# Kernel optimization log

Hardware: AMD Instinct MI355X
Metric: run time of the kernel (lower is better)

## Reference

```python
import jax, jax.numpy as jnp
import numpy as np

EPS = 1e-5

def setup_inputs() -> dict:
    key = jax.random.key(0)
    ks = jax.random.split(key, 8)
    B, T, D, S = 8, 4096, 1024, 64
    return {
        "x": jax.random.normal(ks[0], (B, T, D), dtype=jnp.float32),
        "time_decay": jax.random.normal(ks[1], (S,), dtype=jnp.float32) * 0.1 - 0.5,
        "time_first": jax.random.normal(ks[2], (S,), dtype=jnp.float32) * 0.1,
        "W_key": jax.random.normal(ks[3], (S, D), dtype=jnp.float32) * 0.02,
        "W_value": jax.random.normal(ks[4], (S, D), dtype=jnp.float32) * 0.02,
        "W_output": jax.random.normal(ks[5], (D, S), dtype=jnp.float32) * 0.02,
        "W_shift": jax.random.normal(ks[6], (D, D), dtype=jnp.float32) * 0.02,
        "shift_gate": jnp.ones((D,), dtype=jnp.float32),
        "ln_w": jnp.ones((D,), dtype=jnp.float32),
        "ln_b": jnp.zeros((D,), dtype=jnp.float32),
    }


def _forward(x, time_decay, time_first, W_key, W_value, W_output, W_shift, shift_gate, ln_w, ln_b):
    B, T, D = x.shape
    S = time_decay.shape[0]
    # --- token shift: rotate sequence by shift_len, project, gated blend ---
    shift_len = max(1, int(T * 0.5))
    x_cat = jnp.concatenate([x[:, shift_len:], x[:, :-shift_len]], axis=1)  # (B,T,D)
    gate = jax.nn.sigmoid(shift_gate)
    x_shift = jnp.einsum('btd,ed->bte', x_cat, W_shift) * gate + x * (1.0 - gate)
    # --- layernorm (torch: biased variance, eps=1e-5) ---
    mu = jnp.mean(x_shift, axis=-1, keepdims=True)
    var = jnp.mean(jnp.square(x_shift - mu), axis=-1, keepdims=True)
    xn = (x_shift - mu) * jax.lax.rsqrt(var + EPS) * ln_w + ln_b
    # --- key/value projections and per-step wkv (fully vectorized) ---
    k = jnp.einsum('btd,sd->bts', xn, W_key)    # (B,T,S)
    v = jnp.einsum('btd,sd->bts', xn, W_value)  # (B,T,S)
    wkv = jnp.exp(-jnp.exp(time_first) * jax.nn.sigmoid(k)) * v  # (B,T,S)
    # --- linear recurrence: state = state*w + wkv_t, scanned over T ---
    w = jnp.exp(time_decay)  # (S,)
    def step(state, wkv_t):
        state = state * w + wkv_t
        return state, state
    init = jnp.zeros((B, S), dtype=x.dtype)
    last_state, states = jax.lax.scan(step, init, jnp.swapaxes(wkv, 0, 1))  # states: (T,B,S)
    states = jnp.swapaxes(states, 0, 1)  # (B,T,S)
    # --- batched output projection (applied per-step in torch; same math) ---
    output = jnp.einsum('bts,ds->btd', states, W_output)  # (B,T,D)
    return output, last_state


def reference(x, time_decay, time_first, W_key, W_value, W_output, W_shift, shift_gate, ln_w, ln_b):
    out, last_state = _forward(x, time_decay, time_first, W_key, W_value, W_output, W_shift, shift_gate, ln_w, ln_b)
    return out, jax.lax.stop_gradient(last_state)
```

## Files before the change

kernel.cpp:

```cpp
#include <hip/hip_runtime.h>
#include <stdint.h>

#define B_ 8
#define T_ 4096
#define D_ 1024
#define S_ 64
#define N_ 32768
#define OUT_ELEMS 33554432
#define NCHK 128
#define CHKL 32

typedef __attribute__((ext_vector_type(8))) short bf16x8;
typedef __attribute__((ext_vector_type(8))) unsigned short u16x8;
typedef __attribute__((ext_vector_type(4))) float f32x4;

__device__ __forceinline__ uint16_t f2bf(float f) {
    union { float f; uint32_t u; } v; v.f = f;
    uint32_t r = v.u + 0x7FFFu + ((v.u >> 16) & 1u);
    return (uint16_t)(r >> 16);
}
__device__ __forceinline__ float bf2f(uint16_t h) {
    union { uint32_t u; float f; } v; v.u = ((uint32_t)h) << 16;
    return v.f;
}

#define GLOAD_LDS16(gp, lp)                                             \
    __builtin_amdgcn_global_load_lds(                                   \
        (const __attribute__((address_space(1))) void*)(gp),            \
        (__attribute__((address_space(3))) void*)(lp), 16, 0, 0)

__global__ void prep(const float* __restrict__ x,
                     const float* __restrict__ Wsf, const float* __restrict__ Wkf,
                     const float* __restrict__ Wvf, const float* __restrict__ Wof,
                     const float* __restrict__ sg, const float* __restrict__ tf,
                     const float* __restrict__ lnw, const float* __restrict__ lnb,
                     uint16_t* __restrict__ xb, uint16_t* __restrict__ Wsb,
                     uint16_t* __restrict__ Wkvb, uint16_t* __restrict__ Wob,
                     float* __restrict__ gbuf, float* __restrict__ efirst,
                     float* __restrict__ ucvec)
{
    __shared__ float red[4];
    const int blk = blockIdx.x, tid = threadIdx.x;
    if (blk < 2048) {
        for (int i = blk * 256 + tid; i < OUT_ELEMS / 4; i += 2048 * 256) {
            float4 v = ((const float4*)x)[i];
            ushort4 o;
            o.x = f2bf(v.x); o.y = f2bf(v.y); o.z = f2bf(v.z); o.w = f2bf(v.w);
            ((ushort4*)xb)[i] = o;
        }
        return;
    }
    if (blk < 3298) {
        int i = (blk - 2048) * 256 + tid;
        const float* src; uint16_t* dst; int j; bool fold = false;
        if (i < 262144) { src = Wsf; dst = Wsb; j = i; }
        else if (i < 278528) { src = Wkf; dst = Wkvb; j = i - 262144; fold = true; }
        else if (i < 294912) { src = Wvf; dst = Wkvb + 65536; j = i - 278528; fold = true; }
        else if (i < 311296) { src = Wof; dst = Wob; j = i - 294912; }
        else if (i < 311552) {
            j = i - 311296;
            float4 v = ((const float4*)sg)[j];
            float4 g;
            g.x = 1.f / (1.f + __expf(-v.x)); g.y = 1.f / (1.f + __expf(-v.y));
            g.z = 1.f / (1.f + __expf(-v.z)); g.w = 1.f / (1.f + __expf(-v.w));
            ((float4*)gbuf)[j] = g;
            return;
        } else if (i < 311568) {
            j = i - 311552;
            float4 v = ((const float4*)tf)[j];
            float4 e;
            e.x = __expf(v.x); e.y = __expf(v.y); e.z = __expf(v.z); e.w = __expf(v.w);
            ((float4*)efirst)[j] = e;
            return;
        } else return;
        float4 v = ((const float4*)src)[j];
        if (fold) {
            float4 l = ((const float4*)lnw)[j & 255];
            v.x *= l.x; v.y *= l.y; v.z *= l.z; v.w *= l.w;
        }
        ushort4 o;
        o.x = f2bf(v.x); o.y = f2bf(v.y); o.z = f2bf(v.z); o.w = f2bf(v.w);
        ((ushort4*)dst)[j] = o;
        return;
    }
    {
        int b2 = blk - 3298;
        int which = b2 >> 6, s = b2 & 63;
        const float* W = (which < 2) ? Wkf : Wvf;
        const float* L = (which & 1) ? lnb : lnw;
        float4 wv = ((const float4*)W)[s * 256 + tid];
        float4 lv = ((const float4*)L)[tid];
        float p = wv.x * lv.x + wv.y * lv.y + wv.z * lv.z + wv.w * lv.w;
#pragma unroll
        for (int off = 32; off; off >>= 1) p += __shfl_xor(p, off);
        if ((tid & 63) == 0) red[tid >> 6] = p;
        __syncthreads();
        if (tid == 0) ucvec[which * 64 + s] = red[0] + red[1] + red[2] + red[3];
    }
}

__global__ __launch_bounds__(512, 2) void k1_shift_gemm(
    const uint16_t* __restrict__ xb, const uint16_t* __restrict__ Wsb,
    const float* __restrict__ gbuf, uint16_t* __restrict__ xs)
{
    __shared__ char sh[131072];

    const int tid = threadIdx.x;
    const int w = tid >> 6, lane = tid & 63, quad = lane >> 4, l16 = lane & 15;
    const int wm = w >> 2, wn = w & 3;
    const int w8 = w * 8;

    const int lin = blockIdx.x;
    const int idx = lin >> 3;
    const int nt = idx & 3;
    const int mt = (lin & 7) * 16 + (idx >> 2);
    const int m0 = mt * 256, n0 = nt * 256;
    const int m0x = m0 ^ 2048;

    const int arow = w8 + (lane >> 3);
    const int scg  = ((lane & 7) ^ ((lane >> 3) & 7)) * 8;
    const uint16_t* aBase = xb  + (size_t)(m0x + arow) * D_ + scg;
    const uint16_t* bBase = Wsb + (size_t)(n0  + arow) * D_ + scg;

    const int swz0 = ((quad) ^ (l16 & 7)) * 8;
    const int swz1 = ((4 + quad) ^ (l16 & 7)) * 8;
    const int aRowBase = wm * 128 + l16;
    const int bRowBase = wn * 64 + l16;

    f32x4 acc[8][4];
#pragma unroll
    for (int i = 0; i < 8; ++i)
#pragma unroll
        for (int j = 0; j < 4; ++j) acc[i][j] = (f32x4){0.f, 0.f, 0.f, 0.f};

    {
        uint16_t (*A0)[64] = (uint16_t(*)[64])(sh);
        uint16_t (*B0)[64] = (uint16_t(*)[64])(sh + 32768);
#pragma unroll
        for (int c = 0; c < 4; ++c) {
            GLOAD_LDS16(aBase + (size_t)(c * 64) * D_, &A0[c * 64 + w8][0]);
            GLOAD_LDS16(bBase + (size_t)(c * 64) * D_, &B0[c * 64 + w8][0]);
        }
    }
    asm volatile("s_waitcnt vmcnt(0)" ::: "memory");
    __builtin_amdgcn_s_barrier();

#pragma unroll 1
    for (int t = 0; t < 16; ++t) {
        const int c = t & 1, o = c ^ 1;
        uint16_t (*Ac)[64] = (uint16_t(*)[64])(sh + c * 65536);
        uint16_t (*Bc)[64] = (uint16_t(*)[64])(sh + c * 65536 + 32768);
        uint16_t (*Ao)[64] = (uint16_t(*)[64])(sh + o * 65536);
        uint16_t (*Bo)[64] = (uint16_t(*)[64])(sh + o * 65536 + 32768);
        const int kb1 = (t + 1) * 64;

#pragma unroll
        for (int ks = 0; ks < 2; ++ks) {
            const int swz = ks ? swz1 : swz0;
            bf16x8 a[8], b[4];
#pragma unroll
            for (int mf = 0; mf < 8; ++mf)
                a[mf] = *(const bf16x8*)&Ac[aRowBase + mf * 16][swz];
#pragma unroll
            for (int nf = 0; nf < 4; ++nf)
                b[nf] = *(const bf16x8*)&Bc[bRowBase + nf * 16][swz];
            if (ks == 0 && t < 15) {
#pragma unroll
                for (int cc = 0; cc < 4; ++cc) {
                    GLOAD_LDS16(aBase + (size_t)(cc * 64) * D_ + kb1,
                                &Ao[cc * 64 + w8][0]);
                    GLOAD_LDS16(bBase + (size_t)(cc * 64) * D_ + kb1,
                                &Bo[cc * 64 + w8][0]);
                }
            }
            if (ks == 1 && t < 15) {
                asm volatile("s_waitcnt vmcnt(0)" ::: "memory");
            }
            __builtin_amdgcn_s_barrier();
            __builtin_amdgcn_s_setprio(1);
#pragma unroll
            for (int mf = 0; mf < 8; ++mf)
#pragma unroll
                for (int nf = 0; nf < 4; ++nf)
                    acc[mf][nf] = __builtin_amdgcn_mfma_f32_16x16x32_bf16(
                        a[mf], b[nf], acc[mf][nf], 0, 0, 0);
            __builtin_amdgcn_s_setprio(0);
        }
    }

    float (*epi)[260] = (float(*)[260])sh;
    const int row = tid >> 3;
    const int c0 = (tid & 7) * 32;
#pragma unroll
    for (int mb = 0; mb < 4; ++mb) {
        __syncthreads();
        if (wm == (mb >> 1)) {
#pragma unroll
            for (int mf = 0; mf < 4; ++mf)
#pragma unroll
                for (int nf = 0; nf < 4; ++nf)
#pragma unroll
                    for (int r = 0; r < 4; ++r)
                        epi[mf * 16 + quad * 4 + r][wn * 64 + nf * 16 + l16] =
                            acc[(mb & 1) * 4 + mf][nf][r];
        }
        __syncthreads();
        const int grow = m0 + mb * 64 + row;
        const uint16_t* xrow = xb + (size_t)grow * D_ + n0 + c0;
        uint16_t* orow = xs + (size_t)grow * D_ + n0 + c0;
#pragma unroll
        for (int c4 = 0; c4 < 8; ++c4) {
            float4 g4 = ((const float4*)(gbuf + n0 + c0))[c4];
            ushort4 xh = ((const ushort4*)xrow)[c4];
            const float* e = &epi[row][c0 + c4 * 4];
            ushort4 o;
            o.x = f2bf(e[0] * g4.x + bf2f(xh.x) * (1.f - g4.x));
            o.y = f2bf(e[1] * g4.y + bf2f(xh.y) * (1.f - g4.y));
            o.z = f2bf(e[2] * g4.z + bf2f(xh.z) * (1.f - g4.z));
            o.w = f2bf(e[3] * g4.w + bf2f(xh.w) * (1.f - g4.w));
            ((ushort4*)orow)[c4] = o;
        }
    }
}

__global__ __launch_bounds__(256) void k3_kv(
    const uint16_t* __restrict__ xsb, const uint16_t* __restrict__ Wkvb,
    const float* __restrict__ efirst, const float* __restrict__ ucvec,
    float* __restrict__ wkv)
{
    __shared__ char sh[34816];
    uint16_t (*As)[64] = (uint16_t(*)[64])sh;
    uint16_t (*Bs)[64] = (uint16_t(*)[64])(sh + 8192);
    float (*epi)[132] = (float(*)[132])sh;
    float* ssh = (float*)(sh + 33792);
    float* qsh = (float*)(sh + 34048);

    const int tid = threadIdx.x;
    const int w = tid >> 6, lane = tid & 63, quad = lane >> 4, l16 = lane & 15;
    const int wm = w >> 1, wn = w & 1;
    const int m0 = blockIdx.x * 64;

    const int lrow = w * 8 + (lane >> 3);
    const int scg  = ((lane & 7) ^ ((lane >> 3) & 7)) * 8;
    const uint16_t* aG = xsb + (size_t)(m0 + lrow) * D_ + scg;
    const uint16_t* bG = Wkvb + (size_t)lrow * D_ + scg;

    f32x4 acc[2][4];
#pragma unroll
    for (int i = 0; i < 2; ++i)
#pragma unroll
        for (int j = 0; j < 4; ++j) acc[i][j] = (f32x4){0.f, 0.f, 0.f, 0.f};
    f32x4 accs[2], accq[2];
#pragma unroll
    for (int i = 0; i < 2; ++i) {
        accs[i] = (f32x4){0.f, 0.f, 0.f, 0.f};
        accq[i] = (f32x4){0.f, 0.f, 0.f, 0.f};
    }
    bf16x8 ones;
#pragma unroll
    for (int j = 0; j < 8; ++j) ones[j] = (short)0x3F80;

    for (int k0 = 0; k0 < D_; k0 += 64) {
        __syncthreads();
#pragma unroll
        for (int i = 0; i < 2; ++i)
            GLOAD_LDS16(aG + k0 + (size_t)(i * 32) * D_, &As[w * 8 + i * 32][0]);
#pragma unroll
        for (int i = 0; i < 4; ++i)
            GLOAD_LDS16(bG + k0 + (size_t)(i * 32) * D_, &Bs[w * 8 + i * 32][0]);
        __syncthreads();
#pragma unroll
        for (int ks = 0; ks < 2; ++ks) {
            bf16x8 a[2], b[4];
#pragma unroll
            for (int i = 0; i < 2; ++i)
                a[i] = *(const bf16x8*)&As[wm * 32 + i * 16 + l16]
                                         [(((ks * 4 + quad) ^ (l16 & 7)) * 8)];
#pragma unroll
            for (int j = 0; j < 4; ++j)
                b[j] = *(const bf16x8*)&Bs[wn * 64 + j * 16 + l16]
                                         [(((ks * 4 + quad) ^ (l16 & 7)) * 8)];
#pragma unroll
            for (int i = 0; i < 2; ++i)
#pragma unroll
                for (int j = 0; j < 4; ++j)
                    acc[i][j] = __builtin_amdgcn_mfma_f32_16x16x32_bf16(
                        a[i], b[j], acc[i][j], 0, 0, 0);
            if (wn == 0) {
#pragma unroll
                for (int i = 0; i < 2; ++i) {
                    accs[i] = __builtin_amdgcn_mfma_f32_16x16x32_bf16(
                        a[i], ones, accs[i], 0, 0, 0);
                    accq[i] = __builtin_amdgcn_mfma_f32_16x16x32_bf16(
                        a[i], a[i], accq[i], 0, 0, 0);
                }
            }
        }
    }

    if (wn == 0) {
#pragma unroll
        for (int i = 0; i < 2; ++i) {
            if (l16 == 0) {
#pragma unroll
                for (int r = 0; r < 4; ++r)
                    ssh[wm * 32 + i * 16 + quad * 4 + r] = accs[i][r];
            }
            if ((l16 >> 2) == quad)
                qsh[wm * 32 + i * 16 + l16] = accq[i][l16 & 3];
        }
    }

    __syncthreads();
#pragma unroll
    for (int i = 0; i < 2; ++i)
#pragma unroll
        for (int j = 0; j < 4; ++j)
#pragma unroll
            for (int r = 0; r < 4; ++r)
                epi[wm * 32 + i * 16 + quad * 4 + r][wn * 64 + j * 16 + l16] =
                    acc[i][j][r];
    __syncthreads();

    const int row = tid >> 2, s0 = (tid & 3) * 16;
    const float mu = ssh[row] * (1.f / (float)D_);
    const float var = qsh[row] * (1.f / (float)D_) - mu * mu;
    const float rstd = rsqrtf(var + 1e-5f);
    float* dst = wkv + (size_t)(m0 + row) * S_ + s0;
#pragma unroll
    for (int c4 = 0; c4 < 4; ++c4) {
        float4 kk = *(const float4*)&epi[row][s0 + c4 * 4];
        float4 vv = *(const float4*)&epi[row][64 + s0 + c4 * 4];
        float4 uk4 = *(const float4*)(ucvec + 0 * 64 + s0 + c4 * 4);
        float4 ck4 = *(const float4*)(ucvec + 1 * 64 + s0 + c4 * 4);
        float4 uv4 = *(const float4*)(ucvec + 2 * 64 + s0 + c4 * 4);
        float4 cv4 = *(const float4*)(ucvec + 3 * 64 + s0 + c4 * 4);
        float4 ef = ((const float4*)(efirst + s0))[c4];
        float kx = rstd * (kk.x - mu * uk4.x) + ck4.x;
        float ky = rstd * (kk.y - mu * uk4.y) + ck4.y;
        float kz = rstd * (kk.z - mu * uk4.z) + ck4.z;
        float kw = rstd * (kk.w - mu * uk4.w) + ck4.w;
        float vx = rstd * (vv.x - mu * uv4.x) + cv4.x;
        float vy = rstd * (vv.y - mu * uv4.y) + cv4.y;
        float vz = rstd * (vv.z - mu * uv4.z) + cv4.z;
        float vw = rstd * (vv.w - mu * uv4.w) + cv4.w;
        float4 o;
        o.x = __expf(-ef.x / (1.f + __expf(-kx))) * vx;
        o.y = __expf(-ef.y / (1.f + __expf(-ky))) * vy;
        o.z = __expf(-ef.z / (1.f + __expf(-kz))) * vz;
        o.w = __expf(-ef.w / (1.f + __expf(-kw))) * vw;
        *(float4*)(dst + c4 * 4) = o;
    }
}

__global__ void k4a(const float* __restrict__ wkv,
                    const float* __restrict__ time_decay,
                    float* __restrict__ part)
{
    const int s = threadIdx.x;
    const int bc = blockIdx.x;
    const int b = bc >> 7, c = bc & (NCHK - 1);
    float w = expf(time_decay[s]);
    const float* src = wkv + ((size_t)b * T_ + c * CHKL) * S_ + s;
    float st = 0.f;
#pragma unroll
    for (int t = 0; t < CHKL; ++t) st = st * w + src[(size_t)t * S_];
    part[(size_t)bc * S_ + s] = st;
}
__global__ void k4bc(const float* __restrict__ wkv,
                     const float* __restrict__ time_decay,
                     const float* __restrict__ part,
                     uint16_t* __restrict__ stb,
                     float* __restrict__ last_state)
{
    const int s = threadIdx.x;
    const int bc = blockIdx.x;
    const int b = bc >> 7, c = bc & (NCHK - 1);
    const float td = time_decay[s];
    const float w = expf(td);
    const float wL = expf(td * (float)CHKL);
    const float* pp = part + (size_t)b * NCHK * S_ + s;
    float cin = 0.f;
#pragma unroll 4
    for (int j = 0; j < c; ++j) cin = cin * wL + pp[(size_t)j * S_];
    const float* src = wkv + ((size_t)b * T_ + c * CHKL) * S_ + s;
    uint16_t* dst = stb + ((size_t)b * T_ + c * CHKL) * S_ + s;
    float st = cin;
#pragma unroll
    for (int t = 0; t < CHKL; ++t) {
        st = st * w + src[(size_t)t * S_];
        dst[(size_t)t * S_] = f2bf(st);
    }
    if (c == NCHK - 1) last_state[b * S_ + s] = st;
}

__global__ __launch_bounds__(256) void k5_out(
    const uint16_t* __restrict__ st, const uint16_t* __restrict__ Wob,
    float* __restrict__ out)
{
    __shared__ float epi[128][68];
    const int tid = threadIdx.x;
    const int w = tid >> 6, lane = tid & 63, quad = lane >> 4, l16 = lane & 15;
    const int wm = w >> 1, wn = w & 1;
    const int m0b = blockIdx.y * 128;
    const int n0b = blockIdx.x * 128;

    f32x4 acc[4][4];
#pragma unroll
    for (int i = 0; i < 4; ++i)
#pragma unroll
        for (int j = 0; j < 4; ++j) acc[i][j] = (f32x4){0.f, 0.f, 0.f, 0.f};

#pragma unroll
    for (int k = 0; k < S_; k += 32) {
        bf16x8 a[4], b[4];
#pragma unroll
        for (int i = 0; i < 4; ++i)
            a[i] = *(const bf16x8*)(st + (size_t)(m0b + wm * 64 + i * 16 + l16) * S_ + k + quad * 8);
#pragma unroll
        for (int i = 0; i < 4; ++i)
            b[i] = *(const bf16x8*)(Wob + (size_t)(n0b + wn * 64 + i * 16 + l16) * S_ + k + quad * 8);
#pragma unroll
        for (int i = 0; i < 4; ++i)
#pragma unroll
            for (int j = 0; j < 4; ++j)
                acc[i][j] = __builtin_amdgcn_mfma_f32_16x16x32_bf16(
                    a[i], b[j], acc[i][j], 0, 0, 0);
    }

    const int row = tid >> 1;
    const int c0 = (tid & 1) * 32;
#pragma unroll
    for (int h = 0; h < 2; ++h) {
        __syncthreads();
        if (wn == h) {
#pragma unroll
            for (int i = 0; i < 4; ++i)
#pragma unroll
                for (int j = 0; j < 4; ++j)
#pragma unroll
                    for (int r = 0; r < 4; ++r)
                        epi[wm * 64 + i * 16 + quad * 4 + r][j * 16 + l16] =
                            acc[i][j][r];
        }
        __syncthreads();
        float* dst = out + (size_t)(m0b + row) * D_ + n0b + h * 64 + c0;
#pragma unroll
        for (int c4 = 0; c4 < 8; ++c4)
            ((float4*)dst)[c4] = *(const float4*)&epi[row][c0 + c4 * 4];
    }
}

extern "C" void kernel_launch(void* const* d_in, const int* in_sizes, int n_in,
                              void* d_out, int out_size, void* d_ws, size_t ws_size,
                              hipStream_t stream) {
    const float* x          = (const float*)d_in[0];
    const float* time_decay = (const float*)d_in[1];
    const float* time_first = (const float*)d_in[2];
    const float* W_key      = (const float*)d_in[3];
    const float* W_value    = (const float*)d_in[4];
    const float* W_output   = (const float*)d_in[5];
    const float* W_shift    = (const float*)d_in[6];
    const float* shift_gate = (const float*)d_in[7];
    const float* ln_w       = (const float*)d_in[8];
    const float* ln_b       = (const float*)d_in[9];
    float* out = (float*)d_out;

    char* ws = (char*)d_ws;
    uint16_t* xb      = (uint16_t*)(ws + 0);
    uint16_t* xs      = (uint16_t*)(ws + 67108864);
    float*    wkv     = (float*)   (ws + 134217728);
    uint16_t* stb     = (uint16_t*)(ws + 142606336);
    uint16_t* Wsb     = (uint16_t*)(ws + 146800640);
    uint16_t* Wkvb    = (uint16_t*)(ws + 148897792);
    uint16_t* Wob     = (uint16_t*)(ws + 149159936);
    float*    part    = (float*)   (ws + 149291008);
    float*    gbuf    = (float*)   (ws + 149815296);
    float*    efirst  = (float*)   (ws + 149819392);
    float*    ucvec   = (float*)   (ws + 149819648);

    prep<<<3554, 256, 0, stream>>>(x, W_shift, W_key, W_value, W_output,
                                   shift_gate, time_first, ln_w, ln_b,
                                   xb, Wsb, Wkvb, Wob, gbuf, efirst, ucvec);
    k1_shift_gemm<<<512, 512, 0, stream>>>(xb, Wsb, gbuf, xs);
    k3_kv<<<512, 256, 0, stream>>>(xs, Wkvb, efirst, ucvec, wkv);
    k4a<<<B_ * NCHK, S_, 0, stream>>>(wkv, time_decay, part);
    k4bc<<<B_ * NCHK, S_, 0, stream>>>(wkv, time_decay, part, stb, out + OUT_ELEMS);
    k5_out<<<dim3(8, 256), 256, 0, stream>>>(stb, Wob, out);
}
```

Measured before the change: 426.7 us.

## Split GEMM K-step into four quadrant MFMA phases with interleaved prefetch loads

Restructures the double-buffered GEMM main loop so each 64-wide K tile is processed as four quadrant phases (A low/high × B low/high). Each phase loads only its fragments from LDS and issues part of the next tile's global-to-LDS loads. The waits on those loads are staggered with partial vmcnt counts. The aim is finer overlap of LDS reads, global prefetch and MFMA work, and fewer registers live at once. The cost is more barriers per iteration, and the hand-tuned vmcnt counts must match the order of outstanding loads or the kernel reads stale data.

```diff
diff --git a/kernel.cpp b/kernel.cpp
--- a/kernel.cpp
+++ b/kernel.cpp
@@ -153,39 +153,106 @@
         uint16_t (*Ao)[64] = (uint16_t(*)[64])(sh + o * 65536);
         uint16_t (*Bo)[64] = (uint16_t(*)[64])(sh + o * 65536 + 32768);
         const int kb1 = (t + 1) * 64;
-
-#pragma unroll
-        for (int ks = 0; ks < 2; ++ks) {
-            const int swz = ks ? swz1 : swz0;
-            bf16x8 a[8], b[4];
-#pragma unroll
-            for (int mf = 0; mf < 8; ++mf)
-                a[mf] = *(const bf16x8*)&Ac[aRowBase + mf * 16][swz];
-#pragma unroll
-            for (int nf = 0; nf < 4; ++nf)
-                b[nf] = *(const bf16x8*)&Bc[bRowBase + nf * 16][swz];
-            if (ks == 0 && t < 15) {
-#pragma unroll
-                for (int cc = 0; cc < 4; ++cc) {
-                    GLOAD_LDS16(aBase + (size_t)(cc * 64) * D_ + kb1,
-                                &Ao[cc * 64 + w8][0]);
-                    GLOAD_LDS16(bBase + (size_t)(cc * 64) * D_ + kb1,
-                                &Bo[cc * 64 + w8][0]);
-                }
-            }
-            if (ks == 1 && t < 15) {
-                asm volatile("s_waitcnt vmcnt(0)" ::: "memory");
-            }
-            __builtin_amdgcn_s_barrier();
-            __builtin_amdgcn_s_setprio(1);
-#pragma unroll
-            for (int mf = 0; mf < 8; ++mf)
-#pragma unroll
-                for (int nf = 0; nf < 4; ++nf)
+        const bool st = (t < 15);
+
+        bf16x8 aL[4][2], aH[4][2], bL[2][2], bH[2][2];
+
+#pragma unroll
+        for (int mf = 0; mf < 4; ++mf) {
+            aL[mf][0] = *(const bf16x8*)&Ac[aRowBase + mf * 16][swz0];
+            aL[mf][1] = *(const bf16x8*)&Ac[aRowBase + mf * 16][swz1];
+        }
+#pragma unroll
+        for (int nf = 0; nf < 2; ++nf) {
+            bL[nf][0] = *(const bf16x8*)&Bc[bRowBase + nf * 16][swz0];
+            bL[nf][1] = *(const bf16x8*)&Bc[bRowBase + nf * 16][swz1];
+        }
+        if (st) {
+            GLOAD_LDS16(aBase + (size_t)(0 * 64) * D_ + kb1, &Ao[0 * 64 + w8][0]);
+            GLOAD_LDS16(aBase + (size_t)(2 * 64) * D_ + kb1, &Ao[2 * 64 + w8][0]);
+        }
+        __builtin_amdgcn_s_barrier();
+        asm volatile("s_waitcnt lgkmcnt(0)" ::: "memory");
+        __builtin_amdgcn_sched_barrier(0);
+        __builtin_amdgcn_s_setprio(1);
+#pragma unroll
+        for (int mf = 0; mf < 4; ++mf)
+#pragma unroll
+            for (int nf = 0; nf < 2; ++nf)
+#pragma unroll
+                for (int ks = 0; ks < 2; ++ks)
                     acc[mf][nf] = __builtin_amdgcn_mfma_f32_16x16x32_bf16(
-                        a[mf], b[nf], acc[mf][nf], 0, 0, 0);
-            __builtin_amdgcn_s_setprio(0);
-        }
+                        aL[mf][ks], bL[nf][ks], acc[mf][nf], 0, 0, 0);
+        __builtin_amdgcn_s_setprio(0);
+        __builtin_amdgcn_s_barrier();
+
+#pragma unroll
+        for (int nf = 0; nf < 2; ++nf) {
+            bH[nf][0] = *(const bf16x8*)&Bc[bRowBase + (2 + nf) * 16][swz0];
+            bH[nf][1] = *(const bf16x8*)&Bc[bRowBase + (2 + nf) * 16][swz1];
+        }
+        if (st) {
+            GLOAD_LDS16(bBase + (size_t)(0 * 64) * D_ + kb1, &Bo[0 * 64 + w8][0]);
+            GLOAD_LDS16(bBase + (size_t)(1 * 64) * D_ + kb1, &Bo[1 * 64 + w8][0]);
+        }
+        __builtin_amdgcn_s_barrier();
+        asm volatile("s_waitcnt lgkmcnt(0)" ::: "memory");
+        __builtin_amdgcn_sched_barrier(0);
+        __builtin_amdgcn_s_setprio(1);
+#pragma unroll
+        for (int mf = 0; mf < 4; ++mf)
+#pragma unroll
+            for (int nf = 0; nf < 2; ++nf)
+#pragma unroll
+                for (int ks = 0; ks < 2; ++ks)
+                    acc[mf][2 + nf] = __builtin_amdgcn_mfma_f32_16x16x32_bf16(
+                        aL[mf][ks], bH[nf][ks], acc[mf][2 + nf], 0, 0, 0);
+        __builtin_amdgcn_s_setprio(0);
+        if (st) { asm volatile("s_waitcnt vmcnt(4)" ::: "memory"); }
+        else    { asm volatile("s_waitcnt vmcnt(0)" ::: "memory"); }
+        __builtin_amdgcn_s_barrier();
+
+#pragma unroll
+        for (int mf = 0; mf < 4; ++mf) {
+            aH[mf][0] = *(const bf16x8*)&Ac[aRowBase + (4 + mf) * 16][swz0];
+            aH[mf][1] = *(const bf16x8*)&Ac[aRowBase + (4 + mf) * 16][swz1];
+        }
+        if (st) {
+            GLOAD_LDS16(bBase + (size_t)(2 * 64) * D_ + kb1, &Bo[2 * 64 + w8][0]);
+            GLOAD_LDS16(bBase + (size_t)(3 * 64) * D_ + kb1, &Bo[3 * 64 + w8][0]);
+        }
+        __builtin_amdgcn_s_barrier();
+        asm volatile("s_waitcnt lgkmcnt(0)" ::: "memory");
+        __builtin_amdgcn_sched_barrier(0);
+        __builtin_amdgcn_s_setprio(1);
+#pragma unroll
+        for (int mf = 0; mf < 4; ++mf)
+#pragma unroll
+            for (int nf = 0; nf < 2; ++nf)
+#pragma unroll
+                for (int ks = 0; ks < 2; ++ks)
+                    acc[4 + mf][nf] = __builtin_amdgcn_mfma_f32_16x16x32_bf16(
+                        aH[mf][ks], bL[nf][ks], acc[4 + mf][nf], 0, 0, 0);
+        __builtin_amdgcn_s_setprio(0);
+        __builtin_amdgcn_s_barrier();
+
+        if (st) {
+            GLOAD_LDS16(aBase + (size_t)(1 * 64) * D_ + kb1, &Ao[1 * 64 + w8][0]);
+            GLOAD_LDS16(aBase + (size_t)(3 * 64) * D_ + kb1, &Ao[3 * 64 + w8][0]);
+        }
+        __builtin_amdgcn_s_barrier();
+        __builtin_amdgcn_s_setprio(1);
+#pragma unroll
+        for (int mf = 0; mf < 4; ++mf)
+#pragma unroll
+            for (int nf = 0; nf < 2; ++nf)
+#pragma unroll
+                for (int ks = 0; ks < 2; ++ks)
+                    acc[4 + mf][2 + nf] = __builtin_amdgcn_mfma_f32_16x16x32_bf16(
+                        aH[mf][ks], bH[nf][ks], acc[4 + mf][2 + nf], 0, 0, 0);
+        __builtin_amdgcn_s_setprio(0);
+        if (st) { asm volatile("s_waitcnt vmcnt(2)" ::: "memory"); }
+        __builtin_amdgcn_s_barrier();
     }
 
     float (*epi)[260] = (float(*)[260])sh;
```

After: 431.8 us. No clear change (+1.2%).

## Fuse chunked scan into kv and output-projection kernels, dropping separate scan launches

Applied to the files above, without the earlier changes.

Chunk-local partial scan sums are now computed inside k3_kv from its LDS-staged wkv tile, which removes the k4a launch and its global re-read of wkv. The second scan pass (prefix over chunk partials plus the intra-chunk scan) moves into k5_out, where each block writes bf16 states into a swizzled LDS tile instead of a global stb buffer. This removes two kernel launches and the stb round trip through memory. The cost is that the scan is recomputed by each of the 8 column blocks, each wave walks a serial prefix of up to 127 partials, and k3_kv uses more shared memory.

```diff
diff --git a/kernel.cpp b/kernel.cpp
--- a/kernel.cpp
+++ b/kernel.cpp
@@ -226,14 +226,16 @@
 __global__ __launch_bounds__(256) void k3_kv(
     const uint16_t* __restrict__ xsb, const uint16_t* __restrict__ Wkvb,
     const float* __restrict__ efirst, const float* __restrict__ ucvec,
-    float* __restrict__ wkv)
+    const float* __restrict__ time_decay,
+    float* __restrict__ wkv, float* __restrict__ part)
 {
-    __shared__ char sh[34816];
+    __shared__ char sh[52224];
     uint16_t (*As)[64] = (uint16_t(*)[64])sh;
     uint16_t (*Bs)[64] = (uint16_t(*)[64])(sh + 8192);
     float (*epi)[132] = (float(*)[132])sh;
     float* ssh = (float*)(sh + 33792);
     float* qsh = (float*)(sh + 34048);
+    float (*wsh)[68] = (float(*)[68])(sh + 34816);
 
     const int tid = threadIdx.x;
     const int w = tid >> 6, lane = tid & 63, quad = lane >> 4, l16 = lane & 15;
@@ -350,61 +352,60 @@
         o.z = __expf(-ef.z / (1.f + __expf(-kz))) * vz;
         o.w = __expf(-ef.w / (1.f + __expf(-kw))) * vw;
         *(float4*)(dst + c4 * 4) = o;
-    }
-}
-
-__global__ void k4a(const float* __restrict__ wkv,
-                    const float* __restrict__ time_decay,
-                    float* __restrict__ part)
+        *(float4*)&wsh[row][s0 + c4 * 4] = o;
+    }
+
+    __syncthreads();
+    if (tid < 128) {
+        const int ch = tid >> 6, s = tid & 63;
+        const float w1 = expf(time_decay[s]);
+        float st = 0.f;
+#pragma unroll
+        for (int t = 0; t < CHKL; ++t)
+            st = st * w1 + wsh[ch * CHKL + t][s];
+        const int b = m0 >> 12;
+        const int gc = ((m0 & 4095) >> 5) + ch;
+        part[((size_t)b * NCHK + gc) * S_ + s] = st;
+    }
+}
+
+__global__ __launch_bounds__(256) void k5_out(
+    const float* __restrict__ wkv, const float* __restrict__ part,
+    const float* __restrict__ time_decay, const uint16_t* __restrict__ Wob,
+    float* __restrict__ out, float* __restrict__ last_state)
 {
-    const int s = threadIdx.x;
-    const int bc = blockIdx.x;
-    const int b = bc >> 7, c = bc & (NCHK - 1);
-    float w = expf(time_decay[s]);
-    const float* src = wkv + ((size_t)b * T_ + c * CHKL) * S_ + s;
-    float st = 0.f;
-#pragma unroll
-    for (int t = 0; t < CHKL; ++t) st = st * w + src[(size_t)t * S_];
-    part[(size_t)bc * S_ + s] = st;
-}
-__global__ void k4bc(const float* __restrict__ wkv,
-                     const float* __restrict__ time_decay,
-                     const float* __restrict__ part,
-                     uint16_t* __restrict__ stb,
-                     float* __restrict__ last_state)
-{
-    const int s = threadIdx.x;
-    const int bc = blockIdx.x;
-    const int b = bc >> 7, c = bc & (NCHK - 1);
-    const float td = time_decay[s];
-    const float w = expf(td);
-    const float wL = expf(td * (float)CHKL);
-    const float* pp = part + (size_t)b * NCHK * S_ + s;
-    float cin = 0.f;
-#pragma unroll 4
-    for (int j = 0; j < c; ++j) cin = cin * wL + pp[(size_t)j * S_];
-    const float* src = wkv + ((size_t)b * T_ + c * CHKL) * S_ + s;
-    uint16_t* dst = stb + ((size_t)b * T_ + c * CHKL) * S_ + s;
-    float st = cin;
-#pragma unroll
-    for (int t = 0; t < CHKL; ++t) {
-        st = st * w + src[(size_t)t * S_];
-        dst[(size_t)t * S_] = f2bf(st);
-    }
-    if (c == NCHK - 1) last_state[b * S_ + s] = st;
-}
-
-__global__ __launch_bounds__(256) void k5_out(
-    const uint16_t* __restrict__ st, const uint16_t* __restrict__ Wob,
-    float* __restrict__ out)
-{
-    __shared__ float epi[128][68];
+    __shared__ char sh[34816];
+    uint16_t (*stS)[64] = (uint16_t(*)[64])sh;
+    float (*epi)[68] = (float(*)[68])sh;
+
     const int tid = threadIdx.x;
     const int w = tid >> 6, lane = tid & 63, quad = lane >> 4, l16 = lane & 15;
     const int wm = w >> 1, wn = w & 1;
     const int m0b = blockIdx.y * 128;
     const int n0b = blockIdx.x * 128;
 
+    {
+        const int b = m0b >> 12;
+        const int c = ((m0b & 4095) >> 5) + w;
+        const float td = time_decay[lane];
+        const float w1 = expf(td);
+        const float wL = expf(td * (float)CHKL);
+        const float* pp = part + (size_t)b * NCHK * S_ + lane;
+        float cin = 0.f;
+        for (int j = 0; j < c; ++j) cin = cin * wL + pp[(size_t)j * S_];
+        const float* src = wkv + (size_t)(m0b + w * CHKL) * S_ + lane;
+        float st = cin;
+#pragma unroll
+        for (int t = 0; t < CHKL; ++t) {
+            st = st * w1 + src[(size_t)t * S_];
+            const int row = w * CHKL + t;
+            stS[row][(((lane >> 3) ^ (row & 7)) << 3) | (lane & 7)] = f2bf(st);
+        }
+        if (n0b == 0 && c == NCHK - 1)
+            last_state[b * S_ + lane] = st;
+    }
+    __syncthreads();
+
     f32x4 acc[4][4];
 #pragma unroll
     for (int i = 0; i < 4; ++i)
@@ -415,8 +416,11 @@
     for (int k = 0; k < S_; k += 32) {
         bf16x8 a[4], b[4];
 #pragma unroll
-        for (int i = 0; i < 4; ++i)
-            a[i] = *(const bf16x8*)(st + (size_t)(m0b + wm * 64 + i * 16 + l16) * S_ + k + quad * 8);
+        for (int i = 0; i < 4; ++i) {
+            const int row = wm * 64 + i * 16 + l16;
+            a[i] = *(const bf16x8*)&stS[row]
+                       [((((k >> 3) + quad) ^ (l16 & 7)) * 8)];
+        }
 #pragma unroll
         for (int i = 0; i < 4; ++i)
             b[i] = *(const bf16x8*)(Wob + (size_t)(n0b + wn * 64 + i * 16 + l16) * S_ + k + quad * 8);
@@ -470,7 +474,6 @@
     uint16_t* xb      = (uint16_t*)(ws + 0);
     uint16_t* xs      = (uint16_t*)(ws + 67108864);
     float*    wkv     = (float*)   (ws + 134217728);
-    uint16_t* stb     = (uint16_t*)(ws + 142606336);
     uint16_t* Wsb     = (uint16_t*)(ws + 146800640);
     uint16_t* Wkvb    = (uint16_t*)(ws + 148897792);
     uint16_t* Wob     = (uint16_t*)(ws + 149159936);
@@ -483,8 +486,8 @@
                                    shift_gate, time_first, ln_w, ln_b,
                                    xb, Wsb, Wkvb, Wob, gbuf, efirst, ucvec);
     k1_shift_gemm<<<512, 512, 0, stream>>>(xb, Wsb, gbuf, xs);
-    k3_kv<<<512, 256, 0, stream>>>(xs, Wkvb, efirst, ucvec, wkv);
-    k4a<<<B_ * NCHK, S_, 0, stream>>>(wkv, time_decay, part);
-    k4bc<<<B_ * NCHK, S_, 0, stream>>>(wkv, time_decay, part, stb, out + OUT_ELEMS);
-    k5_out<<<dim3(8, 256), 256, 0, stream>>>(stb, Wob, out);
-}
+    k3_kv<<<512, 256, 0, stream>>>(xs, Wkvb, efirst, ucvec, time_decay,
+                                   wkv, part);
+    k5_out<<<dim3(8, 256), 256, 0, stream>>>(wkv, part, time_decay, Wob,
+                                             out, out + OUT_ELEMS);
+}
```

New measurement: 434.7 us. About the same (+1.9%).

## Double-buffer k3 GEMM with 128-row tiles and fuse chunk-partial scan into it

Applied to the files above, without the earlier changes.

The key/value projection kernel now handles 128 rows per block with a double-buffered LDS pipeline. The next K-slice is prefetched while MFMAs run on the current one, and s_setprio raises priority around the MFMA section. The per-chunk partial recurrence that k4a computed is now done in k3's epilogue from LDS, so k4a and its launch plus its re-read of wkv are removed. This costs more LDS and registers per block and leaves half as many blocks (256) to fill the GPU.

```diff
diff --git a/kernel.cpp b/kernel.cpp
--- a/kernel.cpp
+++ b/kernel.cpp
@@ -226,33 +226,37 @@
 __global__ __launch_bounds__(256) void k3_kv(
     const uint16_t* __restrict__ xsb, const uint16_t* __restrict__ Wkvb,
     const float* __restrict__ efirst, const float* __restrict__ ucvec,
-    float* __restrict__ wkv)
+    const float* __restrict__ time_decay,
+    float* __restrict__ wkv, float* __restrict__ part)
 {
-    __shared__ char sh[34816];
-    uint16_t (*As)[64] = (uint16_t(*)[64])sh;
-    uint16_t (*Bs)[64] = (uint16_t(*)[64])(sh + 8192);
+    __shared__ char sh[68608];
     float (*epi)[132] = (float(*)[132])sh;
-    float* ssh = (float*)(sh + 33792);
-    float* qsh = (float*)(sh + 34048);
+    float* ssh = (float*)(sh + 67584);
 
     const int tid = threadIdx.x;
     const int w = tid >> 6, lane = tid & 63, quad = lane >> 4, l16 = lane & 15;
     const int wm = w >> 1, wn = w & 1;
-    const int m0 = blockIdx.x * 64;
-
-    const int lrow = w * 8 + (lane >> 3);
+    const int w8 = w * 8;
+    const int m0 = blockIdx.x * 128;
+
+    const int arow = w8 + (lane >> 3);
     const int scg  = ((lane & 7) ^ ((lane >> 3) & 7)) * 8;
-    const uint16_t* aG = xsb + (size_t)(m0 + lrow) * D_ + scg;
-    const uint16_t* bG = Wkvb + (size_t)lrow * D_ + scg;
-
-    f32x4 acc[2][4];
-#pragma unroll
-    for (int i = 0; i < 2; ++i)
+    const uint16_t* aBase = xsb + (size_t)(m0 + arow) * D_ + scg;
+    const uint16_t* bBase = Wkvb + (size_t)arow * D_ + scg;
+
+    const int swz0 = ((quad) ^ (l16 & 7)) * 8;
+    const int swz1 = ((4 + quad) ^ (l16 & 7)) * 8;
+    const int aRowBase = wm * 64 + l16;
+    const int bRowBase = wn * 64 + l16;
+
+    f32x4 acc[4][4];
+#pragma unroll
+    for (int i = 0; i < 4; ++i)
 #pragma unroll
         for (int j = 0; j < 4; ++j) acc[i][j] = (f32x4){0.f, 0.f, 0.f, 0.f};
-    f32x4 accs[2], accq[2];
-#pragma unroll
-    for (int i = 0; i < 2; ++i) {
+    f32x4 accs[4], accq[4];
+#pragma unroll
+    for (int i = 0; i < 4; ++i) {
         accs[i] = (f32x4){0.f, 0.f, 0.f, 0.f};
         accq[i] = (f32x4){0.f, 0.f, 0.f, 0.f};
     }
@@ -260,75 +264,102 @@
 #pragma unroll
     for (int j = 0; j < 8; ++j) ones[j] = (short)0x3F80;
 
-    for (int k0 = 0; k0 < D_; k0 += 64) {
-        __syncthreads();
-#pragma unroll
-        for (int i = 0; i < 2; ++i)
-            GLOAD_LDS16(aG + k0 + (size_t)(i * 32) * D_, &As[w * 8 + i * 32][0]);
-#pragma unroll
-        for (int i = 0; i < 4; ++i)
-            GLOAD_LDS16(bG + k0 + (size_t)(i * 32) * D_, &Bs[w * 8 + i * 32][0]);
-        __syncthreads();
+    {
+        uint16_t (*A0)[64] = (uint16_t(*)[64])(sh);
+        uint16_t (*B0)[64] = (uint16_t(*)[64])(sh + 16384);
+#pragma unroll
+        for (int c = 0; c < 4; ++c) {
+            GLOAD_LDS16(aBase + (size_t)(c * 32) * D_, &A0[c * 32 + w8][0]);
+            GLOAD_LDS16(bBase + (size_t)(c * 32) * D_, &B0[c * 32 + w8][0]);
+        }
+    }
+    asm volatile("s_waitcnt vmcnt(0)" ::: "memory");
+    __builtin_amdgcn_s_barrier();
+
+#pragma unroll 1
+    for (int t = 0; t < 16; ++t) {
+        const int c = t & 1, o = c ^ 1;
+        uint16_t (*Ac)[64] = (uint16_t(*)[64])(sh + c * 32768);
+        uint16_t (*Bc)[64] = (uint16_t(*)[64])(sh + c * 32768 + 16384);
+        uint16_t (*Ao)[64] = (uint16_t(*)[64])(sh + o * 32768);
+        uint16_t (*Bo)[64] = (uint16_t(*)[64])(sh + o * 32768 + 16384);
+        const int kb1 = (t + 1) * 64;
+
 #pragma unroll
         for (int ks = 0; ks < 2; ++ks) {
-            bf16x8 a[2], b[4];
-#pragma unroll
-            for (int i = 0; i < 2; ++i)
-                a[i] = *(const bf16x8*)&As[wm * 32 + i * 16 + l16]
-                                         [(((ks * 4 + quad) ^ (l16 & 7)) * 8)];
-#pragma unroll
-            for (int j = 0; j < 4; ++j)
-                b[j] = *(const bf16x8*)&Bs[wn * 64 + j * 16 + l16]
-                                         [(((ks * 4 + quad) ^ (l16 & 7)) * 8)];
-#pragma unroll
-            for (int i = 0; i < 2; ++i)
-#pragma unroll
-                for (int j = 0; j < 4; ++j)
-                    acc[i][j] = __builtin_amdgcn_mfma_f32_16x16x32_bf16(
-                        a[i], b[j], acc[i][j], 0, 0, 0);
-            if (wn == 0) {
-#pragma unroll
-                for (int i = 0; i < 2; ++i) {
-                    accs[i] = __builtin_amdgcn_mfma_f32_16x16x32_bf16(
-                        a[i], ones, accs[i], 0, 0, 0);
-                    accq[i] = __builtin_amdgcn_mfma_f32_16x16x32_bf16(
-                        a[i], a[i], accq[i], 0, 0, 0);
+            const int swz = ks ? swz1 : swz0;
+            bf16x8 a[4], b[4];
+#pragma unroll
+            for (int mf = 0; mf < 4; ++mf)
+                a[mf] = *(const bf16x8*)&Ac[aRowBase + mf * 16][swz];
+#pragma unroll
+            for (int nf = 0; nf < 4; ++nf)
+                b[nf] = *(const bf16x8*)&Bc[bRowBase + nf * 16][swz];
+            if (ks == 0 && t < 15) {
+#pragma unroll
+                for (int cc = 0; cc < 4; ++cc) {
+                    GLOAD_LDS16(aBase + (size_t)(cc * 32) * D_ + kb1,
+                                &Ao[cc * 32 + w8][0]);
+                    GLOAD_LDS16(bBase + (size_t)(cc * 32) * D_ + kb1,
+                                &Bo[cc * 32 + w8][0]);
                 }
             }
-        }
-    }
-
+            if (ks == 1 && t < 15) {
+                asm volatile("s_waitcnt vmcnt(0)" ::: "memory");
+            }
+            __builtin_amdgcn_s_barrier();
+            __builtin_amdgcn_s_setprio(1);
+#pragma unroll
+            for (int mf = 0; mf < 4; ++mf)
+#pragma unroll
+                for (int nf = 0; nf < 4; ++nf)
+                    acc[mf][nf] = __builtin_amdgcn_mfma_f32_16x16x32_bf16(
+                        a[mf], b[nf], acc[mf][nf], 0, 0, 0);
+            if (wn == 0) {
+#pragma unroll
+                for (int mf = 0; mf < 4; ++mf) {
+                    accs[mf] = __builtin_amdgcn_mfma_f32_16x16x32_bf16(
+                        a[mf], ones, accs[mf], 0, 0, 0);
+                    accq[mf] = __builtin_amdgcn_mfma_f32_16x16x32_bf16(
+                        a[mf], a[mf], accq[mf], 0, 0, 0);
+                }
+            }
+            __builtin_amdgcn_s_setprio(0);
+        }
+    }
+
+    float* qsh = (float*)(sh + 68096);
     if (wn == 0) {
 #pragma unroll
-        for (int i = 0; i < 2; ++i) {
+        for (int mf = 0; mf < 4; ++mf) {
             if (l16 == 0) {
 #pragma unroll
                 for (int r = 0; r < 4; ++r)
-                    ssh[wm * 32 + i * 16 + quad * 4 + r] = accs[i][r];
+                    ssh[wm * 64 + mf * 16 + quad * 4 + r] = accs[mf][r];
             }
             if ((l16 >> 2) == quad)
-                qsh[wm * 32 + i * 16 + l16] = accq[i][l16 & 3];
+                qsh[wm * 64 + mf * 16 + l16] = accq[mf][l16 & 3];
         }
     }
 
     __syncthreads();
 #pragma unroll
-    for (int i = 0; i < 2; ++i)
+    for (int i = 0; i < 4; ++i)
 #pragma unroll
         for (int j = 0; j < 4; ++j)
 #pragma unroll
             for (int r = 0; r < 4; ++r)
-                epi[wm * 32 + i * 16 + quad * 4 + r][wn * 64 + j * 16 + l16] =
+                epi[wm * 64 + i * 16 + quad * 4 + r][wn * 64 + j * 16 + l16] =
                     acc[i][j][r];
     __syncthreads();
 
-    const int row = tid >> 2, s0 = (tid & 3) * 16;
+    const int row = tid >> 1, s0 = (tid & 1) * 32;
     const float mu = ssh[row] * (1.f / (float)D_);
     const float var = qsh[row] * (1.f / (float)D_) - mu * mu;
     const float rstd = rsqrtf(var + 1e-5f);
     float* dst = wkv + (size_t)(m0 + row) * S_ + s0;
 #pragma unroll
-    for (int c4 = 0; c4 < 4; ++c4) {
+    for (int c4 = 0; c4 < 8; ++c4) {
         float4 kk = *(const float4*)&epi[row][s0 + c4 * 4];
         float4 vv = *(const float4*)&epi[row][64 + s0 + c4 * 4];
         float4 uk4 = *(const float4*)(ucvec + 0 * 64 + s0 + c4 * 4);
@@ -350,23 +381,23 @@
         o.z = __expf(-ef.z / (1.f + __expf(-kz))) * vz;
         o.w = __expf(-ef.w / (1.f + __expf(-kw))) * vw;
         *(float4*)(dst + c4 * 4) = o;
-    }
-}
-
-__global__ void k4a(const float* __restrict__ wkv,
-                    const float* __restrict__ time_decay,
-                    float* __restrict__ part)
-{
-    const int s = threadIdx.x;
-    const int bc = blockIdx.x;
-    const int b = bc >> 7, c = bc & (NCHK - 1);
-    float w = expf(time_decay[s]);
-    const float* src = wkv + ((size_t)b * T_ + c * CHKL) * S_ + s;
-    float st = 0.f;
-#pragma unroll
-    for (int t = 0; t < CHKL; ++t) st = st * w + src[(size_t)t * S_];
-    part[(size_t)bc * S_ + s] = st;
-}
+        *(float4*)&epi[row][s0 + c4 * 4] = o;
+    }
+
+    __syncthreads();
+    {
+        const int ch = tid >> 6, s = tid & 63;
+        const float w1 = expf(time_decay[s]);
+        float st = 0.f;
+#pragma unroll
+        for (int t = 0; t < CHKL; ++t)
+            st = st * w1 + epi[ch * CHKL + t][s];
+        const int b = m0 >> 12;
+        const int gc = ((m0 & 4095) >> 5) + ch;
+        part[((size_t)b * NCHK + gc) * S_ + s] = st;
+    }
+}
+
 __global__ void k4bc(const float* __restrict__ wkv,
                      const float* __restrict__ time_decay,
                      const float* __restrict__ part,
@@ -483,8 +514,9 @@
                                    shift_gate, time_first, ln_w, ln_b,
                                    xb, Wsb, Wkvb, Wob, gbuf, efirst, ucvec);
     k1_shift_gemm<<<512, 512, 0, stream>>>(xb, Wsb, gbuf, xs);
-    k3_kv<<<512, 256, 0, stream>>>(xs, Wkvb, efirst, ucvec, wkv);
-    k4a<<<B_ * NCHK, S_, 0, stream>>>(wkv, time_decay, part);
-    k4bc<<<B_ * NCHK, S_, 0, stream>>>(wkv, time_decay, part, stb, out + OUT_ELEMS);
+    k3_kv<<<256, 256, 0, stream>>>(xs, Wkvb, efirst, ucvec, time_decay,
+                                   wkv, part);
+    k4bc<<<B_ * NCHK, S_, 0, stream>>>(wkv, time_decay, part, stb,
+                                       out + OUT_ELEMS);
     k5_out<<<dim3(8, 256), 256, 0, stream>>>(stb, Wob, out);
 }
```

Measured after the change: 427.1 us. No clear change (+0.1%).
